# Optimization experiments

Hardware: AMD Instinct MI355X
Metric: run time of the kernel (lower is better)

## Reference

```python
import jax, jax.numpy as jnp
import numpy as np

V, D, NH, L, T, B = 32000, 1024, 16, 6, 1024, 2
HS = D // NH
EPS = 1e-5


def setup_inputs() -> dict:
    key = jax.random.key(0)
    ks = jax.random.split(key, 20)
    s = 0.02
    inp = {
        'tokens': jax.random.randint(ks[0], (B, T), 0, V),
        'tok_emb': jax.random.normal(ks[1], (V, D), jnp.float32) * s,
        'pos_emb': jax.random.normal(ks[2], (T, D), jnp.float32) * s,
        'Wq': jax.random.normal(ks[3], (L, D, NH, HS), jnp.float32) * s,
        'Wk': jax.random.normal(ks[4], (L, D, NH, HS), jnp.float32) * s,
        'Wv': jax.random.normal(ks[5], (L, D, NH, HS), jnp.float32) * s,
        'Wo': jax.random.normal(ks[6], (L, D, D), jnp.float32) * s,
        'bo': jnp.zeros((L, D), jnp.float32),
        'ln1_s': jnp.ones((L, D), jnp.float32),
        'ln1_b': jnp.zeros((L, D), jnp.float32),
        'ln2_s': jnp.ones((L, D), jnp.float32),
        'ln2_b': jnp.zeros((L, D), jnp.float32),
        'W1': jax.random.normal(ks[7], (L, D, 4 * D), jnp.float32) * s,
        'b1': jnp.zeros((L, 4 * D), jnp.float32),
        'W2': jax.random.normal(ks[8], (L, 4 * D, D), jnp.float32) * s,
        'b2': jnp.zeros((L, D), jnp.float32),
        'lnf_s': jnp.ones((D,), jnp.float32),
        'lnf_b': jnp.zeros((D,), jnp.float32),
        'Wlm': jax.random.normal(ks[9], (D, V), jnp.float32) * s,
        'blm': jnp.zeros((V,), jnp.float32),
    }
    return inp


def _layernorm(x, scale, bias):
    m = jnp.mean(x, axis=-1, keepdims=True)
    v = jnp.mean(jnp.square(x - m), axis=-1, keepdims=True)
    return (x - m) * jax.lax.rsqrt(v + EPS) * scale + bias


def reference(tokens, tok_emb, pos_emb, Wq, Wk, Wv, Wo, bo,
              ln1_s, ln1_b, ln2_s, ln2_b, W1, b1, W2, b2,
              lnf_s, lnf_b, Wlm, blm):
    x = tok_emb[tokens] + pos_emb[None, :, :]  # [B,T,D]
    causal = jnp.tril(jnp.ones((T, T), bool))
    scale = HS ** -0.5
    for l in range(L):
        h = _layernorm(x, ln1_s[l], ln1_b[l])
        q = jnp.einsum('btd,dhe->bhte', h, Wq[l])
        k = jnp.einsum('btd,dhe->bhte', h, Wk[l])
        v = jnp.einsum('btd,dhe->bhte', h, Wv[l])
        wei = jnp.einsum('bhqe,bhke->bhqk', q, k) * scale
        wei = jnp.where(causal, wei, -jnp.inf)
        wei = jax.nn.softmax(wei, axis=-1)
        attn = jnp.einsum('bhqk,bhke->bhqe', wei, v)  # [B,NH,T,HS]
        attn = attn.transpose(0, 2, 1, 3).reshape(B, T, D)
        x = x + attn @ Wo[l] + bo[l]
        h = _layernorm(x, ln2_s[l], ln2_b[l])
        x = x + jax.nn.relu(h @ W1[l] + b1[l]) @ W2[l] + b2[l]
    x = _layernorm(x, lnf_s, lnf_b)
    logits = x @ Wlm + blm  # [B,T,V]
    return logits
```

## Files before the change

kernel.cpp:

```cpp
#include <hip/hip_runtime.h>
#include <hip/hip_bf16.h>
#include <stdint.h>

#define L_LAYERS 6
#define D_MODEL  1024
#define N_HEAD   16
#define H_SZ     64
#define T_SEQ    1024
#define B_BATCH  2
#define M_ROWS   2048
#define V_VOCAB  32000

typedef __attribute__((ext_vector_type(8))) short bf16x8;
typedef __attribute__((ext_vector_type(4))) short bf16x4;
typedef __attribute__((ext_vector_type(4))) float floatx4;

static __device__ __forceinline__ short f2bf(float f) {
  __hip_bfloat16 h = __float2bfloat16(f);
  return *reinterpret_cast<short*>(&h);
}

static __device__ __forceinline__ void lds_cp16(const void* g, void* l) {
  __builtin_amdgcn_global_load_lds(
      (const __attribute__((address_space(1))) uint32_t*)g,
// ... 20 lines not shown
    int r = r0 + (p << 4);
    float4 v = *(const float4*)(ip + (size_t)r * C + c0);
    tile[r][c0] = v.x; tile[r][c0 + 1] = v.y; tile[r][c0 + 2] = v.z; tile[r][c0 + 3] = v.w;
  }
  __syncthreads();
  short* op = out + (size_t)(ct * 64) * R + rt * 64;
#pragma unroll
  for (int p = 0; p < 4; ++p) {
    int c = r0 + (p << 4);
    bf16x4 s;
    s.x = f2bf(tile[c0 + 0][c]);
    s.y = f2bf(tile[c0 + 1][c]);
    s.z = f2bf(tile[c0 + 2][c]);
    s.w = f2bf(tile[c0 + 3][c]);
    *(bf16x4*)(op + (size_t)c * R + c0) = s;
  }
}

__global__ __launch_bounds__(256) void embedln_kernel(const int* __restrict__ tokens,
                                                      const float* __restrict__ tok_emb,
                                                      const float* __restrict__ pos_emb,
                                                      float* __restrict__ x,
                                                      const float* __restrict__ sc,
                                                      const float* __restrict__ bi,
                                                      short* __restrict__ out) {
  int row = blockIdx.x, tid = threadIdx.x;
  int t = row & 1023;
  int tok = tokens[row];
  int c = tid << 2;
  float4 e = *(const float4*)(tok_emb + (size_t)tok * 1024 + c);
  float4 p = *(const float4*)(pos_emb + (size_t)t * 1024 + c);
  float4 v; v.x = e.x + p.x; v.y = e.y + p.y; v.z = e.z + p.z; v.w = e.w + p.w;
  *(float4*)(x + (size_t)row * 1024 + c) = v;
  float s = v.x + v.y + v.z + v.w;
  float q = v.x * v.x + v.y * v.y + v.z * v.z + v.w * v.w;
#pragma unroll
  for (int off = 32; off > 0; off >>= 1) {
    s += __shfl_xor(s, off);
    q += __shfl_xor(q, off);
  }
  __shared__ float rs[4], rq[4];
  if ((tid & 63) == 0) { rs[tid >> 6] = s; rq[tid >> 6] = q; }
  __syncthreads();
  s = rs[0] + rs[1] + rs[2] + rs[3];
  q = rq[0] + rq[1] + rq[2] + rq[3];
  float mean = s * (1.f / 1024.f);
  float var = q * (1.f / 1024.f) - mean * mean;
  float rstd = rsqrtf(var + 1e-5f);
  float4 g = *(const float4*)(sc + c);
  float4 bb = *(const float4*)(bi + c);
  bf16x4 o4;
  o4.x = f2bf((v.x - mean) * rstd * g.x + bb.x);
  o4.y = f2bf((v.y - mean) * rstd * g.y + bb.y);
  o4.z = f2bf((v.z - mean) * rstd * g.z + bb.z);
  o4.w = f2bf((v.w - mean) * rstd * g.w + bb.w);
  *(bf16x4*)(out + (size_t)row * 1024 + c) = o4;
}

__global__ __launch_bounds__(256) void lnred_kernel(float* __restrict__ xio,
                                                    const float* __restrict__ P0,
                                                    const float* __restrict__ P1,
                                                    const float* __restrict__ gb,
                                                    const float* __restrict__ sc,
                                                    const float* __restrict__ bi,
                                                    short* __restrict__ out) {
  int row = blockIdx.x, tid = threadIdx.x;
  int c = tid << 2;
  size_t base = (size_t)row * 1024 + c;
  float4 v = *(const float4*)(xio + base);
  float4 p0 = *(const float4*)(P0 + base);
  float4 p1 = *(const float4*)(P1 + base);
  float4 gv = *(const float4*)(gb + c);
  v.x += p0.x + p1.x + gv.x;
  v.y += p0.y + p1.y + gv.y;
  v.z += p0.z + p1.z + gv.z;
  v.w += p0.w + p1.w + gv.w;
  *(float4*)(xio + base) = v;
  float s = v.x + v.y + v.z + v.w;
  float q = v.x * v.x + v.y * v.y + v.z * v.z + v.w * v.w;
#pragma unroll
  for (int off = 32; off > 0; off >>= 1) {
    s += __shfl_xor(s, off);
    q += __shfl_xor(q, off);
  }
  __shared__ float rs[4], rq[4];
  if ((tid & 63) == 0) { rs[tid >> 6] = s; rq[tid >> 6] = q; }
  __syncthreads();
  s = rs[0] + rs[1] + rs[2] + rs[3];
  q = rq[0] + rq[1] + rq[2] + rq[3];
  float mean = s * (1.f / 1024.f);
  float var = q * (1.f / 1024.f) - mean * mean;
  float rstd = rsqrtf(var + 1e-5f);
  float4 g = *(const float4*)(sc + c);
  float4 bb = *(const float4*)(bi + c);
  bf16x4 o4;
  o4.x = f2bf((v.x - mean) * rstd * g.x + bb.x);
  o4.y = f2bf((v.y - mean) * rstd * g.y + bb.y);
  o4.z = f2bf((v.z - mean) * rstd * g.z + bb.z);
  o4.w = f2bf((v.w - mean) * rstd * g.w + bb.w);
  *(bf16x4*)(out + (size_t)row * 1024 + c) = o4;
}

__global__ __launch_bounds__(256) void lnred4_kernel(float* __restrict__ xio,
                                                     const float* __restrict__ P01,
                                                     const float* __restrict__ P23,
                                                     const float* __restrict__ gb,
                                                     const float* __restrict__ sc,
                                                     const float* __restrict__ bi,
                                                     short* __restrict__ out) {
  const size_t MN = (size_t)M_ROWS * 1024;
// ... 4 lines not shown
  float4 p0 = *(const float4*)(P01 + base);
  float4 p1 = *(const float4*)(P01 + MN + base);
  float4 p2 = *(const float4*)(P23 + base);
  float4 p3 = *(const float4*)(P23 + MN + base);
  float4 gv = *(const float4*)(gb + c);
  v.x += p0.x + p1.x + p2.x + p3.x + gv.x;
  v.y += p0.y + p1.y + p2.y + p3.y + gv.y;
  v.z += p0.z + p1.z + p2.z + p3.z + gv.z;
  v.w += p0.w + p1.w + p2.w + p3.w + gv.w;
  *(float4*)(xio + base) = v;
  float s = v.x + v.y + v.z + v.w;
  float q = v.x * v.x + v.y * v.y + v.z * v.z + v.w * v.w;
#pragma unroll
  for (int off = 32; off > 0; off >>= 1) {
    s += __shfl_xor(s, off);
    q += __shfl_xor(q, off);
  }
  __shared__ float rs[4], rq[4];
  if ((tid & 63) == 0) { rs[tid >> 6] = s; rq[tid >> 6] = q; }
  __syncthreads();
  s = rs[0] + rs[1] + rs[2] + rs[3];
  q = rq[0] + rq[1] + rq[2] + rq[3];
  float mean = s * (1.f / 1024.f);
  float var = q * (1.f / 1024.f) - mean * mean;
  float rstd = rsqrtf(var + 1e-5f);
  float4 g = *(const float4*)(sc + c);
  float4 bb = *(const float4*)(bi + c);
  bf16x4 o4;
  o4.x = f2bf((v.x - mean) * rstd * g.x + bb.x);
  o4.y = f2bf((v.y - mean) * rstd * g.y + bb.y);
  o4.z = f2bf((v.z - mean) * rstd * g.z + bb.z);
  o4.w = f2bf((v.w - mean) * rstd * g.w + bb.w);
  *(bf16x4*)(out + (size_t)row * 1024 + c) = o4;
}

__global__ __launch_bounds__(256) void gemm3sk_kernel(const short* __restrict__ A,
                                                      const short* __restrict__ Bt,
                                                      float* __restrict__ Pout,
                                                      int K, int N) {
  constexpr int ABY = 64 * 128;
  constexpr int BBY = 128 * 128;
  extern __shared__ char smem[];
  char* Asm = smem;
  char* Bsm = smem + 3 * ABY;
  const int NB = N >> 7;
  int nwg = 64 * NB;
  int bid = blockIdx.x;
  int wgid = (bid & 7) * (nwg >> 3) + (bid >> 3);
  int half = wgid >= (nwg >> 1);
  int w2 = wgid - half * (nwg >> 1);
  int bn = w2 >> 5, bm = w2 & 31;
  int kbase = half * (K >> 1);
  Pout += (size_t)half * M_ROWS * N;
  int tid = threadIdx.x;
  int lane = tid & 63, w = tid >> 6;
  int lr = lane & 15, lg = lane >> 4;
  int wn = w & 1, wm = w >> 1;

  const floatx4 FZ = {0.f, 0.f, 0.f, 0.f};
  floatx4 acc[2][4];
#pragma unroll
  for (int m = 0; m < 2; ++m)
#pragma unroll
    for (int n = 0; n < 4; ++n) acc[m][n] = FZ;

  size_t aoff[2], boff[4];
  {
    int rr = tid >> 3;
    int g = (tid & 7) ^ (rr & 7);
#pragma unroll
    for (int i = 0; i < 2; ++i)
      aoff[i] = (size_t)(bm * 64 + i * 32 + rr) * K + kbase + g * 8;
#pragma unroll
    for (int i = 0; i < 4; ++i)
      boff[i] = (size_t)(bn * 128 + i * 32 + rr) * K + kbase + g * 8;
  }

#define STA3(b, k0)                                                        \
  _Pragma("unroll") for (int i = 0; i < 2; ++i)                            \
    lds_cp16(A + aoff[i] + (k0), Asm + (b) * ABY + i * 4096 + tid * 16);
#define STB3(b, k0)                                                        \
  _Pragma("unroll") for (int i = 0; i < 4; ++i)                            \
    lds_cp16(Bt + boff[i] + (k0), Bsm + (b) * BBY + i * 4096 + tid * 16);
#define LDA3(b, kh)                                                        \
  _Pragma("unroll") for (int f = 0; f < 2; ++f) {                          \
    int lrow = wm * 32 + f * 16 + lr;                                      \
    af[f] = *(const bf16x8*)(Asm + (b) * ABY + lrow * 128 +                \
                             (((((kh) << 2) + lg) ^ (lrow & 7)) << 4));    \
  }
#define LDB3(b, kh)                                                        \
  _Pragma("unroll") for (int n = 0; n < 4; ++n) {                          \
    int lcol = wn * 64 + n * 16 + lr;                                      \
    bfr[n] = *(const bf16x8*)(Bsm + (b) * BBY + lcol * 128 +               \
                              (((((kh) << 2) + lg) ^ (lcol & 7)) << 4));   \
  }
#define MFMA3                                                              \
  __builtin_amdgcn_s_setprio(1);                                           \
  _Pragma("unroll") for (int f = 0; f < 2; ++f)                            \
  _Pragma("unroll") for (int n = 0; n < 4; ++n)                            \
    acc[f][n] = __builtin_amdgcn_mfma_f32_16x16x32_bf16(af[f], bfr[n],     \
                                                        acc[f][n], 0, 0, 0);\
  __builtin_amdgcn_s_setprio(0);

  const int nt = (K >> 1) >> 6;
  STA3(0, 0); STB3(0, 0);
  STA3(1, 64); STB3(1, 64);
  WVM(6);
  BARR;

  int cbuf = 0, sbuf = 2;
  for (int t = 0; t < nt; ++t) {
    bf16x8 af[2], bfr[4];
    bool pre = (t + 2 < nt);
    int k2 = (t + 2) << 6;
    if (pre) { STA3(sbuf, k2); }
    LDA3(cbuf, 0); LDB3(cbuf, 0);
    MFMA3;
    if (pre) { STB3(sbuf, k2); }
    LDA3(cbuf, 1); LDB3(cbuf, 1);
    MFMA3;
    if (pre) { WVM(6); } else { WVM(0); }
    BARR;
    cbuf = (cbuf == 2) ? 0 : cbuf + 1;
    sbuf = (sbuf == 2) ? 0 : sbuf + 1;
  }

#pragma unroll
  for (int n = 0; n < 4; ++n) {
    int col = (bn << 7) + wn * 64 + (n << 4) + lr;
#pragma unroll
    for (int m = 0; m < 2; ++m) {
      int row0 = bm * 64 + wm * 32 + (m << 4) + (lg << 2);
#pragma unroll
      for (int r = 0; r < 4; ++r)
        Pout[(size_t)(row0 + r) * N + col] = acc[m][n][r];
    }
  }
#undef STA3
#undef STB3
#undef LDA3
#undef LDB3
#undef MFMA3
}

template <bool BIAS, bool RELU, bool OUTBF16>
__global__ __launch_bounds__(512) void gemmw_kernel(const short* __restrict__ A,
                                                    const short* __restrict__ Bt,
                                                    const float* __restrict__ bias,
                                                    void* __restrict__ Cout,
                                                    int K, int N) {
  constexpr int ABY = 128 * 128;
  constexpr int BBY = 256 * 128;
  extern __shared__ char smem[];
  char* Asm = smem;
  char* Bsm = smem + 3 * ABY;
  const int NB = N >> 8;
  int nwg = 16 * NB;
  int bid = blockIdx.x;
  int wgid = (bid & 7) * (nwg >> 3) + (bid >> 3);
  int bn = wgid >> 4, bm = wgid & 15;
  int tid = threadIdx.x;
  int lane = tid & 63, w = tid >> 6;
  int lr = lane & 15, lg = lane >> 4;
  int wm = w >> 2, wn = w & 3;

  const floatx4 FZ = {0.f, 0.f, 0.f, 0.f};
  floatx4 acc[4][4];
#pragma unroll
  for (int m = 0; m < 4; ++m)
#pragma unroll
    for (int n = 0; n < 4; ++n) acc[m][n] = FZ;

  size_t aoff[2], boff[4];
  {
    int rr = tid >> 3;
    int g = (tid & 7) ^ (rr & 7);
#pragma unroll
    for (int i = 0; i < 2; ++i)
      aoff[i] = (size_t)(bm * 128 + i * 64 + rr) * K + g * 8;
#pragma unroll
    for (int i = 0; i < 4; ++i)
      boff[i] = (size_t)(bn * 256 + i * 64 + rr) * K + g * 8;
// ... 26 lines not shown
  __builtin_amdgcn_s_setprio(0);

  const int nt = K >> 6;
  STAW(0, 0); STBW(0, 0);
  STAW(1, 64); STBW(1, 64);
  WVM(6);
  BARR;

  int cbuf = 0, sbuf = 2;
  for (int t = 0; t < nt; ++t) {
    bf16x8 af[4], bfr[4];
    bool pre = (t + 2 < nt);
    int k2 = (t + 2) << 6;
    if (pre) { STAW(sbuf, k2); }
    LDAW(cbuf, 0); LDBW(cbuf, 0);
    MFMAW;
    if (pre) { STBW(sbuf, k2); }
    LDAW(cbuf, 1); LDBW(cbuf, 1);
    MFMAW;
    if (pre) { WVM(6); } else { WVM(0); }
    BARR;
    cbuf = (cbuf == 2) ? 0 : cbuf + 1;
    sbuf = (sbuf == 2) ? 0 : sbuf + 1;
  }

#pragma unroll
  for (int n = 0; n < 4; ++n) {
    int col = (bn << 8) + wn * 64 + (n << 4) + lr;
    float bv = 0.f;
    if (BIAS) bv = bias[col];
#pragma unroll
    for (int m = 0; m < 4; ++m) {
      int row0 = bm * 128 + wm * 64 + (m << 4) + (lg << 2);
#pragma unroll
      for (int r = 0; r < 4; ++r) {
        size_t idx = (size_t)(row0 + r) * N + col;
        float val = acc[m][n][r] + bv;
        if (RELU) val = fmaxf(val, 0.f);
        if (OUTBF16) ((short*)Cout)[idx] = f2bf(val);
        else ((float*)Cout)[idx] = val;
      }
    }
  }
#undef STAW
#undef STBW
#undef LDAW
#undef LDBW
#undef MFMAW
}

__global__ __launch_bounds__(512) void gemmwsk_kernel(const short* __restrict__ A,
                                                      const short* __restrict__ Bt,
                                                      float* __restrict__ P01,
                                                      float* __restrict__ P23,
                                                      int K, int N) {
  constexpr int ABY = 128 * 128;
  constexpr int BBY = 256 * 128;
  extern __shared__ char smem[];
  char* Asm = smem;
  char* Bsm = smem + 3 * ABY;
  const int NB = N >> 8;
  int nwg = 16 * NB * 4;
  int bid = blockIdx.x;
  int wgid = (bid & 7) * (nwg >> 3) + (bid >> 3);
  int per = nwg >> 2;
  int part = wgid / per;
  int w2 = wgid - part * per;
  int bn = w2 >> 4, bm = w2 & 15;
  int kbase = part * (K >> 2);
  float* Pout = (part < 2 ? P01 + (size_t)part * M_ROWS * N
                          : P23 + (size_t)(part - 2) * M_ROWS * N);
  int tid = threadIdx.x;
  int lane = tid & 63, w = tid >> 6;
// ... 196 lines not shown
  LDA8(0, 1); LDB8(1);
  MFMA16(0, 1);
  WVM(0);
  BARR;
  LDA8(1, 0);
  MFMA16(1, 0);
  LDA8(1, 1);
  MFMA16(1, 1);

#pragma unroll
  for (int n = 0; n < 4; ++n) {
    int col = (bn << 8) + (wn << 6) + (n << 4) + lr;
    float bv = 0.f;
    if (BIAS) bv = bias[col];
#pragma unroll
    for (int m = 0; m < 8; ++m) {
      int row0 = (bm << 8) + (wm << 7) + (m << 4) + (lg << 2);
#pragma unroll
      for (int r = 0; r < 4; ++r) {
        size_t idx = (size_t)(row0 + r) * N + col;
        float val = acc[m][n][r] + bv;
        if (OUTBF16) ((short*)Cout)[idx] = f2bf(val);
        else ((float*)Cout)[idx] = val;
      }
    }
  }
#undef LDA8
#undef LDB8
#undef MFMA16
#undef STA8
#undef STB8
}

__global__ __launch_bounds__(256) void vt_kernel(const short* __restrict__ qkv,
                                                 short* __restrict__ vt) {
  int bh = blockIdx.x, tt = blockIdx.y;
  int b = bh >> 4, hh = bh & 15;
  __shared__ short tile[64][68];
  int tid = threadIdx.x;
  int r0 = tid >> 4;
  int c4 = (tid & 15) << 2;
  const short* ip = qkv + (size_t)((b << 10) + (tt << 6)) * 3072 + 2048 + (hh << 6);
#pragma unroll
  for (int p = 0; p < 4; ++p) {
    int t = r0 + (p << 4);
    bf16x4 v = *(const bf16x4*)(ip + (size_t)t * 3072 + c4);
    tile[t][c4] = v.x; tile[t][c4 + 1] = v.y; tile[t][c4 + 2] = v.z; tile[t][c4 + 3] = v.w;
  }
  __syncthreads();
  short* op = vt + (size_t)(bh << 6) * 1024 + (tt << 6);
#pragma unroll
  for (int p = 0; p < 4; ++p) {
    int e = r0 + (p << 4);
    bf16x4 sv;
    sv.x = tile[c4 + 0][e];
    sv.y = tile[c4 + 1][e];
    sv.z = tile[c4 + 2][e];
    sv.w = tile[c4 + 3][e];
    *(bf16x4*)(op + (size_t)e * 1024 + c4) = sv;
  }
}

__global__ __launch_bounds__(256) void attn_kernel(const short* __restrict__ qkv,
                                                   const short* __restrict__ vt,
                                                   short* __restrict__ out) {
  int bh = blockIdx.x;
  int qt = blockIdx.y;
  int b = bh >> 4, hh = bh & 15;
  int tid = threadIdx.x;
  int lane = tid & 63, w = tid >> 6;
  int lr = lane & 15, lg = lane >> 4;

  __shared__ short Ks[64 * 64];
  __shared__ short Vs[64 * 64];
  __shared__ short Ps[4][16 * 68];

  const floatx4 FZ = {0.f, 0.f, 0.f, 0.f};
  const short* qb = qkv + (size_t)((b << 10) + (qt << 6) + (w << 4) + lr) * 3072 + (hh << 6);
  bf16x8 qf0 = *(const bf16x8*)(qb + (lg << 3));
  bf16x8 qf1 = *(const bf16x8*)(qb + 32 + (lg << 3));

  floatx4 o[4];
  float mrun[4], lrun[4];
#pragma unroll
  for (int r = 0; r < 4; ++r) { o[r] = FZ; mrun[r] = -3e38f; lrun[r] = 0.f; }

  int sr = lane >> 3;
  int cb = (lane & 7) << 4;
  int csw = cb ^ (sr << 4);
  const short* kB = qkv + (size_t)(b << 10) * 3072 + 1024 + (hh << 6);
  const short* vB = vt + (size_t)(bh << 6) * 1024;

  for (int jt = 0; jt <= qt; ++jt) {
    __syncthreads();
#pragma unroll
    for (int j = 0; j < 2; ++j) {
      int ch = w * 2 + j;
      int row = (ch << 3) + sr;
      lds_cp16(kB + (size_t)((jt << 6) + row) * 3072 + (csw >> 1), (short*)Ks + (ch << 9));
      lds_cp16(vB + (size_t)row * 1024 + (jt << 6) + (csw >> 1), (short*)Vs + (ch << 9));
    }
    __syncthreads();

    const char* KsB = (const char*)Ks;
    const char* VsB = (const char*)Vs;
    floatx4 s[4];
#pragma unroll
    for (int f = 0; f < 4; ++f) {
      int rk = (f << 4) + lr;
      int sw = (rk & 7) << 4;
      bf16x8 kf0 = *(const bf16x8*)(KsB + rk * 128 + ((lg << 4) ^ sw));
      bf16x8 kf1 = *(const bf16x8*)(KsB + rk * 128 + ((64 + (lg << 4)) ^ sw));
      floatx4 t = __builtin_amdgcn_mfma_f32_16x16x32_bf16(qf0, kf0, FZ, 0, 0, 0);
      s[f] = __builtin_amdgcn_mfma_f32_16x16x32_bf16(qf1, kf1, t, 0, 0, 0);
    }

    float p[4][4], mt[4];
    bool diag = (jt == qt);
    int rowloc = (w << 4) + (lg << 2);
#pragma unroll
    for (int r = 0; r < 4; ++r) {
      float m = -3e38f;
#pragma unroll
      for (int f = 0; f < 4; ++f) {
        float sv = s[f][r] * 0.125f;
        if (diag && ((f << 4) + lr > rowloc + r)) sv = -3e38f;
        p[f][r] = sv;
        m = fmaxf(m, sv);
      }
      mt[r] = m;
    }
#pragma unroll
    for (int off = 1; off < 16; off <<= 1) {
#pragma unroll
      for (int r = 0; r < 4; ++r) mt[r] = fmaxf(mt[r], __shfl_xor(mt[r], off));
    }
    float corr[4], psum[4];
#pragma unroll
    for (int r = 0; r < 4; ++r) {
      float mnew = fmaxf(mrun[r], mt[r]);
      corr[r] = __expf(mrun[r] - mnew);
      mrun[r] = mnew;
      float ps = 0.f;
#pragma unroll
      for (int f = 0; f < 4; ++f) {
        float e = __expf(p[f][r] - mnew);
        p[f][r] = e;
        ps += e;
      }
      psum[r] = ps;
    }
#pragma unroll
    for (int off = 1; off < 16; off <<= 1) {
#pragma unroll
      for (int r = 0; r < 4; ++r) psum[r] += __shfl_xor(psum[r], off);
    }
    floatx4 cv;
#pragma unroll
    for (int r = 0; r < 4; ++r) { lrun[r] = lrun[r] * corr[r] + psum[r]; cv[r] = corr[r]; }
#pragma unroll
    for (int f = 0; f < 4; ++f) o[f] *= cv;

    char* PsB = (char*)&Ps[w][0];
#pragma unroll
    for (int f = 0; f < 4; ++f)
#pragma unroll
      for (int r = 0; r < 4; ++r)
        *(short*)(PsB + ((lg << 2) + r) * 136 + (((f << 4) + lr) << 1)) = f2bf(p[f][r]);

#pragma unroll
    for (int kk = 0; kk < 2; ++kk) {
      const char* pb = PsB + lr * 136 + (kk << 6) + (lg << 4);
      union { struct { bf16x4 lo, hi; } h2; bf16x8 v; } pu;
      pu.h2.lo = *(const bf16x4*)pb;
      pu.h2.hi = *(const bf16x4*)(pb + 8);
      bf16x8 pa = pu.v;
#pragma unroll
      for (int f = 0; f < 4; ++f) {
        int rv = (f << 4) + lr;
        int sw = (rv & 7) << 4;
        bf16x8 vf = *(const bf16x8*)(VsB + rv * 128 + ((((kk << 6)) + (lg << 4)) ^ sw));
        o[f] = __builtin_amdgcn_mfma_f32_16x16x32_bf16(pa, vf, o[f], 0, 0, 0);
      }
    }
  }

#pragma unroll
  for (int f = 0; f < 4; ++f) {
#pragma unroll
    for (int r = 0; r < 4; ++r) {
      int row = (qt << 6) + (w << 4) + (lg << 2) + r;
      int col = (hh << 6) + (f << 4) + lr;
      out[(size_t)((b << 10) + row) * 1024 + col] = f2bf(o[f][r] / lrun[r]);
    }
  }
}

extern "C" void kernel_launch(void* const* d_in, const int* in_sizes, int n_in,
                              void* d_out, int out_size, void* d_ws, size_t ws_size,
                              hipStream_t stream) {
  const int*   tokens  = (const int*)d_in[0];
  const float* tok_emb = (const float*)d_in[1];
  const float* pos_emb = (const float*)d_in[2];
  const float* Wq  = (const float*)d_in[3];
  const float* Wk  = (const float*)d_in[4];
  const float* Wv  = (const float*)d_in[5];
  const float* Wo  = (const float*)d_in[6];
  const float* bo  = (const float*)d_in[7];
  const float* ln1s = (const float*)d_in[8];
  const float* ln1b = (const float*)d_in[9];
  const float* ln2s = (const float*)d_in[10];
  const float* ln2b = (const float*)d_in[11];
  const float* W1  = (const float*)d_in[12];
  const float* b1  = (const float*)d_in[13];
  const float* W2  = (const float*)d_in[14];
  const float* b2  = (const float*)d_in[15];
  const float* lnfs = (const float*)d_in[16];
  const float* lnfb = (const float*)d_in[17];
  const float* Wlm = (const float*)d_in[18];
  const float* blm = (const float*)d_in[19];

  short* wqkvT = (short*)d_ws;
  short* woT   = wqkvT + (size_t)L_LAYERS * 3072 * 1024;
  short* w1T   = woT   + (size_t)L_LAYERS * 1024 * 1024;
  short* w2T   = w1T   + (size_t)L_LAYERS * 4096 * 1024;
  short* wlmT  = w2T   + (size_t)L_LAYERS * 1024 * 4096;
  float* x     = (float*)(wlmT + (size_t)V_VOCAB * 1024);
  short* h     = (short*)(x + (size_t)M_ROWS * 1024);
  short* qkv   = h + (size_t)M_ROWS * 1024;
  short* vtb   = qkv + (size_t)M_ROWS * 3072;
  short* attnb = vtb + (size_t)B_BATCH * N_HEAD * H_SZ * T_SEQ;
  short* mid   = attnb + (size_t)M_ROWS * 1024;
  float* psum  = (float*)(mid + (size_t)M_ROWS * 4096);
  float* psum1 = psum + (size_t)M_ROWS * 1024;
  float* psum23 = (float*)qkv;

  dim3 blk(256, 1, 1);

  (void)hipFuncSetAttribute(reinterpret_cast<const void*>(&gemm8_kernel<true, false>),
                            hipFuncAttributeMaxDynamicSharedMemorySize, 131072);
  (void)hipFuncSetAttribute(reinterpret_cast<const void*>(&gemm3sk_kernel),
                            hipFuncAttributeMaxDynamicSharedMemorySize, 73728);
  (void)hipFuncSetAttribute(reinterpret_cast<const void*>(&gemmw_kernel<false, false, true>),
                            hipFuncAttributeMaxDynamicSharedMemorySize, 147456);
  (void)hipFuncSetAttribute(reinterpret_cast<const void*>(&gemmw_kernel<true, true, true>),
                            hipFuncAttributeMaxDynamicSharedMemorySize, 147456);
  (void)hipFuncSetAttribute(reinterpret_cast<const void*>(&gemmwsk_kernel),
                            hipFuncAttributeMaxDynamicSharedMemorySize, 147456);

  transpose_cvt<<<dim3(16, 16, 6), blk, 0, stream>>>(Wq, wqkvT,             1024, 1024, 1048576, 3072 * 1024);
  transpose_cvt<<<dim3(16, 16, 6), blk, 0, stream>>>(Wk, wqkvT + 1048576,   1024, 1024, 1048576, 3072 * 1024);
  transpose_cvt<<<dim3(16, 16, 6), blk, 0, stream>>>(Wv, wqkvT + 2097152,   1024, 1024, 1048576, 3072 * 1024);
  transpose_cvt<<<dim3(16, 16, 6), blk, 0, stream>>>(Wo, woT,               1024, 1024, 1048576, 1048576);
  transpose_cvt<<<dim3(16, 64, 6), blk, 0, stream>>>(W1, w1T,               1024, 4096, 4194304, 4194304);
  transpose_cvt<<<dim3(64, 16, 6), blk, 0, stream>>>(W2, w2T,               4096, 1024, 4194304, 4194304);
  transpose_cvt<<<dim3(16, 500, 1), blk, 0, stream>>>(Wlm, wlmT,            1024, V_VOCAB, 0, 0);

  embedln_kernel<<<M_ROWS, blk, 0, stream>>>(tokens, tok_emb, pos_emb, x, ln1s, ln1b, h);

  for (int l = 0; l < L_LAYERS; ++l) {
    if (l > 0) {
      lnred4_kernel<<<M_ROWS, blk, 0, stream>>>(x, psum, psum23, b2 + (l - 1) * 1024,
                                                ln1s + l * 1024, ln1b + l * 1024, h);
    }
    gemmw_kernel<false, false, true><<<16 * 12, dim3(512, 1, 1), 147456, stream>>>(
        h, wqkvT + (size_t)l * 3072 * 1024, nullptr, qkv, 1024, 3072);
    vt_kernel<<<dim3(32, 16), blk, 0, stream>>>(qkv, vtb);
    attn_kernel<<<dim3(32, 16), blk, 0, stream>>>(qkv, vtb, attnb);
    gemm3sk_kernel<<<64 * 8, blk, 73728, stream>>>(
        attnb, woT + (size_t)l * 1048576, psum, 1024, 1024);
    lnred_kernel<<<M_ROWS, blk, 0, stream>>>(x, psum, psum1, bo + l * 1024,
                                             ln2s + l * 1024, ln2b + l * 1024, h);
    gemmw_kernel<true, true, true><<<16 * 16, dim3(512, 1, 1), 147456, stream>>>(
        h, w1T + (size_t)l * 4194304, b1 + l * 4096, mid, 1024, 4096);
    gemmwsk_kernel<<<16 * 16, dim3(512, 1, 1), 147456, stream>>>(
        mid, w2T + (size_t)l * 4194304, psum, psum23, 4096, 1024);
  }

  lnred4_kernel<<<M_ROWS, blk, 0, stream>>>(x, psum, psum23, b2 + 5 * 1024,
                                            lnfs, lnfb, h);
  gemm8_kernel<true, false><<<dim3(8 * 125), dim3(512, 1, 1), 131072, stream>>>(
      h, wlmT, blm, (float*)d_out, 1024, V_VOCAB);
}
```

Measured before the change: 1.075 ms.

## Double-buffer attention K/V loads, use exp2 softmax, reuse split-K GEMM for Wo

The attention kernel now double-buffers its K and V tiles in LDS. It issues async global-to-LDS copies for the next key block while computing the current one, replacing the two full barriers around each synchronous load. Softmax folds log2(e) into the score scale and uses exp2f instead of __expf. The output projection drops the dedicated 2-way split-K gemm3sk kernel and reuses the wider gemmwsk kernel with 4 K-partials written to psum/psum23, followed by lnred4 instead of lnred. This trades more partial-sum traffic and doubled attention LDS for better latency hiding and fewer distinct kernel variants.

```diff
diff --git a/kernel.cpp b/kernel.cpp
--- a/kernel.cpp
+++ b/kernel.cpp
@@ -76,50 +76,6 @@
   float4 p = *(const float4*)(pos_emb + (size_t)t * 1024 + c);
   float4 v; v.x = e.x + p.x; v.y = e.y + p.y; v.z = e.z + p.z; v.w = e.w + p.w;
   *(float4*)(x + (size_t)row * 1024 + c) = v;
-  float s = v.x + v.y + v.z + v.w;
-  float q = v.x * v.x + v.y * v.y + v.z * v.z + v.w * v.w;
-#pragma unroll
-  for (int off = 32; off > 0; off >>= 1) {
-    s += __shfl_xor(s, off);
-    q += __shfl_xor(q, off);
-  }
-  __shared__ float rs[4], rq[4];
-  if ((tid & 63) == 0) { rs[tid >> 6] = s; rq[tid >> 6] = q; }
-  __syncthreads();
-  s = rs[0] + rs[1] + rs[2] + rs[3];
-  q = rq[0] + rq[1] + rq[2] + rq[3];
-  float mean = s * (1.f / 1024.f);
-  float var = q * (1.f / 1024.f) - mean * mean;
-  float rstd = rsqrtf(var + 1e-5f);
-  float4 g = *(const float4*)(sc + c);
-  float4 bb = *(const float4*)(bi + c);
-  bf16x4 o4;
-  o4.x = f2bf((v.x - mean) * rstd * g.x + bb.x);
-  o4.y = f2bf((v.y - mean) * rstd * g.y + bb.y);
-  o4.z = f2bf((v.z - mean) * rstd * g.z + bb.z);
-  o4.w = f2bf((v.w - mean) * rstd * g.w + bb.w);
-  *(bf16x4*)(out + (size_t)row * 1024 + c) = o4;
-}
-
-__global__ __launch_bounds__(256) void lnred_kernel(float* __restrict__ xio,
-                                                    const float* __restrict__ P0,
-                                                    const float* __restrict__ P1,
-                                                    const float* __restrict__ gb,
-                                                    const float* __restrict__ sc,
-                                                    const float* __restrict__ bi,
-                                                    short* __restrict__ out) {
-  int row = blockIdx.x, tid = threadIdx.x;
-  int c = tid << 2;
-  size_t base = (size_t)row * 1024 + c;
-  float4 v = *(const float4*)(xio + base);
-  float4 p0 = *(const float4*)(P0 + base);
-  float4 p1 = *(const float4*)(P1 + base);
-  float4 gv = *(const float4*)(gb + c);
-  v.x += p0.x + p1.x + gv.x;
-  v.y += p0.y + p1.y + gv.y;
-  v.z += p0.z + p1.z + gv.z;
-  v.w += p0.w + p1.w + gv.w;
-  *(float4*)(xio + base) = v;
   float s = v.x + v.y + v.z + v.w;
   float q = v.x * v.x + v.y * v.y + v.z * v.z + v.w * v.w;
 #pragma unroll
@@ -190,115 +146,6 @@
   o4.z = f2bf((v.z - mean) * rstd * g.z + bb.z);
   o4.w = f2bf((v.w - mean) * rstd * g.w + bb.w);
   *(bf16x4*)(out + (size_t)row * 1024 + c) = o4;
-}
-
-__global__ __launch_bounds__(256) void gemm3sk_kernel(const short* __restrict__ A,
-                                                      const short* __restrict__ Bt,
-                                                      float* __restrict__ Pout,
-                                                      int K, int N) {
-  constexpr int ABY = 64 * 128;
-  constexpr int BBY = 128 * 128;
-  extern __shared__ char smem[];
-  char* Asm = smem;
-  char* Bsm = smem + 3 * ABY;
-  const int NB = N >> 7;
-  int nwg = 64 * NB;
-  int bid = blockIdx.x;
-  int wgid = (bid & 7) * (nwg >> 3) + (bid >> 3);
-  int half = wgid >= (nwg >> 1);
-  int w2 = wgid - half * (nwg >> 1);
-  int bn = w2 >> 5, bm = w2 & 31;
-  int kbase = half * (K >> 1);
-  Pout += (size_t)half * M_ROWS * N;
-  int tid = threadIdx.x;
-  int lane = tid & 63, w = tid >> 6;
-  int lr = lane & 15, lg = lane >> 4;
-  int wn = w & 1, wm = w >> 1;
-
-  const floatx4 FZ = {0.f, 0.f, 0.f, 0.f};
-  floatx4 acc[2][4];
-#pragma unroll
-  for (int m = 0; m < 2; ++m)
-#pragma unroll
-    for (int n = 0; n < 4; ++n) acc[m][n] = FZ;
-
-  size_t aoff[2], boff[4];
-  {
-    int rr = tid >> 3;
-    int g = (tid & 7) ^ (rr & 7);
-#pragma unroll
-    for (int i = 0; i < 2; ++i)
-      aoff[i] = (size_t)(bm * 64 + i * 32 + rr) * K + kbase + g * 8;
-#pragma unroll
-    for (int i = 0; i < 4; ++i)
-      boff[i] = (size_t)(bn * 128 + i * 32 + rr) * K + kbase + g * 8;
-  }
-
-#define STA3(b, k0)                                                        \
-  _Pragma("unroll") for (int i = 0; i < 2; ++i)                            \
-    lds_cp16(A + aoff[i] + (k0), Asm + (b) * ABY + i * 4096 + tid * 16);
-#define STB3(b, k0)                                                        \
-  _Pragma("unroll") for (int i = 0; i < 4; ++i)                            \
-    lds_cp16(Bt + boff[i] + (k0), Bsm + (b) * BBY + i * 4096 + tid * 16);
-#define LDA3(b, kh)                                                        \
-  _Pragma("unroll") for (int f = 0; f < 2; ++f) {                          \
-    int lrow = wm * 32 + f * 16 + lr;                                      \
-    af[f] = *(const bf16x8*)(Asm + (b) * ABY + lrow * 128 +                \
-                             (((((kh) << 2) + lg) ^ (lrow & 7)) << 4));    \
-  }
-#define LDB3(b, kh)                                                        \
-  _Pragma("unroll") for (int n = 0; n < 4; ++n) {                          \
-    int lcol = wn * 64 + n * 16 + lr;                                      \
-    bfr[n] = *(const bf16x8*)(Bsm + (b) * BBY + lcol * 128 +               \
-                              (((((kh) << 2) + lg) ^ (lcol & 7)) << 4));   \
-  }
-#define MFMA3                                                              \
-  __builtin_amdgcn_s_setprio(1);                                           \
-  _Pragma("unroll") for (int f = 0; f < 2; ++f)                            \
-  _Pragma("unroll") for (int n = 0; n < 4; ++n)                            \
-    acc[f][n] = __builtin_amdgcn_mfma_f32_16x16x32_bf16(af[f], bfr[n],     \
-                                                        acc[f][n], 0, 0, 0);\
-  __builtin_amdgcn_s_setprio(0);
-
-  const int nt = (K >> 1) >> 6;
-  STA3(0, 0); STB3(0, 0);
-  STA3(1, 64); STB3(1, 64);
-  WVM(6);
-  BARR;
-
-  int cbuf = 0, sbuf = 2;
-  for (int t = 0; t < nt; ++t) {
-    bf16x8 af[2], bfr[4];
-    bool pre = (t + 2 < nt);
-    int k2 = (t + 2) << 6;
-    if (pre) { STA3(sbuf, k2); }
-    LDA3(cbuf, 0); LDB3(cbuf, 0);
-    MFMA3;
-    if (pre) { STB3(sbuf, k2); }
-    LDA3(cbuf, 1); LDB3(cbuf, 1);
-    MFMA3;
-    if (pre) { WVM(6); } else { WVM(0); }
-    BARR;
-    cbuf = (cbuf == 2) ? 0 : cbuf + 1;
-    sbuf = (sbuf == 2) ? 0 : sbuf + 1;
-  }
-
-#pragma unroll
-  for (int n = 0; n < 4; ++n) {
-    int col = (bn << 7) + wn * 64 + (n << 4) + lr;
-#pragma unroll
-    for (int m = 0; m < 2; ++m) {
-      int row0 = bm * 64 + wm * 32 + (m << 4) + (lg << 2);
-#pragma unroll
-      for (int r = 0; r < 4; ++r)
-        Pout[(size_t)(row0 + r) * N + col] = acc[m][n][r];
-    }
-  }
-#undef STA3
-#undef STB3
-#undef LDA3
-#undef LDB3
-#undef MFMA3
 }
 
 template <bool BIAS, bool RELU, bool OUTBF16>
@@ -706,11 +553,12 @@
   int lane = tid & 63, w = tid >> 6;
   int lr = lane & 15, lg = lane >> 4;
 
-  __shared__ short Ks[64 * 64];
-  __shared__ short Vs[64 * 64];
+  __shared__ short Ks[2][64 * 64];
+  __shared__ short Vs[2][64 * 64];
   __shared__ short Ps[4][16 * 68];
 
   const floatx4 FZ = {0.f, 0.f, 0.f, 0.f};
+  const float C2 = 0.18033688f;
   const short* qb = qkv + (size_t)((b << 10) + (qt << 6) + (w << 4) + lr) * 3072 + (hh << 6);
   bf16x8 qf0 = *(const bf16x8*)(qb + (lg << 3));
   bf16x8 qf1 = *(const bf16x8*)(qb + 32 + (lg << 3));
@@ -726,19 +574,26 @@
   const short* kB = qkv + (size_t)(b << 10) * 3072 + 1024 + (hh << 6);
   const short* vB = vt + (size_t)(bh << 6) * 1024;
 
+#define STKV(jt, bb)                                                       \
+  _Pragma("unroll") for (int j = 0; j < 2; ++j) {                          \
+    int ch = w * 2 + j;                                                    \
+    int row = (ch << 3) + sr;                                              \
+    lds_cp16(kB + (size_t)(((jt) << 6) + row) * 3072 + (csw >> 1),         \
+             (short*)Ks + (bb) * 4096 + (ch << 9));                        \
+    lds_cp16(vB + (size_t)row * 1024 + ((jt) << 6) + (csw >> 1),           \
+             (short*)Vs + (bb) * 4096 + (ch << 9));                        \
+  }
+
+  STKV(0, 0);
+  WVM(0);
+  BARR;
+
+  int buf = 0;
   for (int jt = 0; jt <= qt; ++jt) {
-    __syncthreads();
-#pragma unroll
-    for (int j = 0; j < 2; ++j) {
-      int ch = w * 2 + j;
-      int row = (ch << 3) + sr;
-      lds_cp16(kB + (size_t)((jt << 6) + row) * 3072 + (csw >> 1), (short*)Ks + (ch << 9));
-      lds_cp16(vB + (size_t)row * 1024 + (jt << 6) + (csw >> 1), (short*)Vs + (ch << 9));
-    }
-    __syncthreads();
-
-    const char* KsB = (const char*)Ks;
-    const char* VsB = (const char*)Vs;
+    if (jt < qt) { STKV(jt + 1, buf ^ 1); }
+
+    const char* KsB = (const char*)Ks + (buf << 13);
+    const char* VsB = (const char*)Vs + (buf << 13);
     floatx4 s[4];
 #pragma unroll
     for (int f = 0; f < 4; ++f) {
@@ -758,7 +613,7 @@
       float m = -3e38f;
 #pragma unroll
       for (int f = 0; f < 4; ++f) {
-        float sv = s[f][r] * 0.125f;
+        float sv = s[f][r] * C2;
         if (diag && ((f << 4) + lr > rowloc + r)) sv = -3e38f;
         p[f][r] = sv;
         m = fmaxf(m, sv);
@@ -774,12 +629,12 @@
 #pragma unroll
     for (int r = 0; r < 4; ++r) {
       float mnew = fmaxf(mrun[r], mt[r]);
-      corr[r] = __expf(mrun[r] - mnew);
+      corr[r] = exp2f(mrun[r] - mnew);
       mrun[r] = mnew;
       float ps = 0.f;
 #pragma unroll
       for (int f = 0; f < 4; ++f) {
-        float e = __expf(p[f][r] - mnew);
+        float e = exp2f(p[f][r] - mnew);
         p[f][r] = e;
         ps += e;
       }
@@ -818,7 +673,12 @@
         o[f] = __builtin_amdgcn_mfma_f32_16x16x32_bf16(pa, vf, o[f], 0, 0, 0);
       }
     }
-  }
+
+    WVM(0);
+    BARR;
+    buf ^= 1;
+  }
+#undef STKV
 
 #pragma unroll
   for (int f = 0; f < 4; ++f) {
@@ -867,15 +727,12 @@
   short* attnb = vtb + (size_t)B_BATCH * N_HEAD * H_SZ * T_SEQ;
   short* mid   = attnb + (size_t)M_ROWS * 1024;
   float* psum  = (float*)(mid + (size_t)M_ROWS * 4096);
-  float* psum1 = psum + (size_t)M_ROWS * 1024;
   float* psum23 = (float*)qkv;
 
   dim3 blk(256, 1, 1);
 
   (void)hipFuncSetAttribute(reinterpret_cast<const void*>(&gemm8_kernel<true, false>),
                             hipFuncAttributeMaxDynamicSharedMemorySize, 131072);
-  (void)hipFuncSetAttribute(reinterpret_cast<const void*>(&gemm3sk_kernel),
-                            hipFuncAttributeMaxDynamicSharedMemorySize, 73728);
   (void)hipFuncSetAttribute(reinterpret_cast<const void*>(&gemmw_kernel<false, false, true>),
                             hipFuncAttributeMaxDynamicSharedMemorySize, 147456);
   (void)hipFuncSetAttribute(reinterpret_cast<const void*>(&gemmw_kernel<true, true, true>),
@@ -902,10 +759,10 @@
         h, wqkvT + (size_t)l * 3072 * 1024, nullptr, qkv, 1024, 3072);
     vt_kernel<<<dim3(32, 16), blk, 0, stream>>>(qkv, vtb);
     attn_kernel<<<dim3(32, 16), blk, 0, stream>>>(qkv, vtb, attnb);
-    gemm3sk_kernel<<<64 * 8, blk, 73728, stream>>>(
-        attnb, woT + (size_t)l * 1048576, psum, 1024, 1024);
-    lnred_kernel<<<M_ROWS, blk, 0, stream>>>(x, psum, psum1, bo + l * 1024,
-                                             ln2s + l * 1024, ln2b + l * 1024, h);
+    gemmwsk_kernel<<<16 * 4 * 4, dim3(512, 1, 1), 147456, stream>>>(
+        attnb, woT + (size_t)l * 1048576, psum, psum23, 1024, 1024);
+    lnred4_kernel<<<M_ROWS, blk, 0, stream>>>(x, psum, psum23, bo + l * 1024,
+                                              ln2s + l * 1024, ln2b + l * 1024, h);
     gemmw_kernel<true, true, true><<<16 * 16, dim3(512, 1, 1), 147456, stream>>>(
         h, w1T + (size_t)l * 4194304, b1 + l * 4096, mid, 1024, 4096);
     gemmwsk_kernel<<<16 * 16, dim3(512, 1, 1), 147456, stream>>>(
```

Result: slower. 1.117 ms (+3.9%).

## Double-buffer K/V tiles in attention and switch softmax to exp2

Applied to the files above, without the earlier changes.

The attention kernel now holds two K/V LDS buffers. It issues the async global-to-LDS load for the next key tile before computing on the current one, with a single wait and barrier per iteration in place of two barriers. The softmax scale is folded into log2e so exp2f replaces __expf. This is meant to hide global load latency behind the MFMA work, at the cost of doubled LDS use, which may reduce occupancy.

```diff
diff --git a/kernel.cpp b/kernel.cpp
--- a/kernel.cpp
+++ b/kernel.cpp
@@ -706,11 +706,12 @@
   int lane = tid & 63, w = tid >> 6;
   int lr = lane & 15, lg = lane >> 4;
 
-  __shared__ short Ks[64 * 64];
-  __shared__ short Vs[64 * 64];
+  __shared__ short Ks[2][64 * 64];
+  __shared__ short Vs[2][64 * 64];
   __shared__ short Ps[4][16 * 68];
 
   const floatx4 FZ = {0.f, 0.f, 0.f, 0.f};
+  const float C2 = 0.18033688f;
   const short* qb = qkv + (size_t)((b << 10) + (qt << 6) + (w << 4) + lr) * 3072 + (hh << 6);
   bf16x8 qf0 = *(const bf16x8*)(qb + (lg << 3));
   bf16x8 qf1 = *(const bf16x8*)(qb + 32 + (lg << 3));
@@ -726,19 +727,26 @@
   const short* kB = qkv + (size_t)(b << 10) * 3072 + 1024 + (hh << 6);
   const short* vB = vt + (size_t)(bh << 6) * 1024;
 
+#define STKV(jt, bb)                                                       \
+  _Pragma("unroll") for (int j = 0; j < 2; ++j) {                          \
+    int ch = w * 2 + j;                                                    \
+    int row = (ch << 3) + sr;                                              \
+    lds_cp16(kB + (size_t)(((jt) << 6) + row) * 3072 + (csw >> 1),         \
+             (short*)Ks + (bb) * 4096 + (ch << 9));                        \
+    lds_cp16(vB + (size_t)row * 1024 + ((jt) << 6) + (csw >> 1),           \
+             (short*)Vs + (bb) * 4096 + (ch << 9));                        \
+  }
+
+  STKV(0, 0);
+  WVM(0);
+  BARR;
+
+  int buf = 0;
   for (int jt = 0; jt <= qt; ++jt) {
-    __syncthreads();
-#pragma unroll
-    for (int j = 0; j < 2; ++j) {
-      int ch = w * 2 + j;
-      int row = (ch << 3) + sr;
-      lds_cp16(kB + (size_t)((jt << 6) + row) * 3072 + (csw >> 1), (short*)Ks + (ch << 9));
-      lds_cp16(vB + (size_t)row * 1024 + (jt << 6) + (csw >> 1), (short*)Vs + (ch << 9));
-    }
-    __syncthreads();
-
-    const char* KsB = (const char*)Ks;
-    const char* VsB = (const char*)Vs;
+    if (jt < qt) { STKV(jt + 1, buf ^ 1); }
+
+    const char* KsB = (const char*)Ks + (buf << 13);
+    const char* VsB = (const char*)Vs + (buf << 13);
     floatx4 s[4];
 #pragma unroll
     for (int f = 0; f < 4; ++f) {
@@ -758,7 +766,7 @@
       float m = -3e38f;
 #pragma unroll
       for (int f = 0; f < 4; ++f) {
-        float sv = s[f][r] * 0.125f;
+        float sv = s[f][r] * C2;
         if (diag && ((f << 4) + lr > rowloc + r)) sv = -3e38f;
         p[f][r] = sv;
         m = fmaxf(m, sv);
@@ -774,12 +782,12 @@
 #pragma unroll
     for (int r = 0; r < 4; ++r) {
       float mnew = fmaxf(mrun[r], mt[r]);
-      corr[r] = __expf(mrun[r] - mnew);
+      corr[r] = exp2f(mrun[r] - mnew);
       mrun[r] = mnew;
       float ps = 0.f;
 #pragma unroll
       for (int f = 0; f < 4; ++f) {
-        float e = __expf(p[f][r] - mnew);
+        float e = exp2f(p[f][r] - mnew);
         p[f][r] = e;
         ps += e;
       }
@@ -818,7 +826,12 @@
         o[f] = __builtin_amdgcn_mfma_f32_16x16x32_bf16(pa, vf, o[f], 0, 0, 0);
       }
     }
-  }
+
+    WVM(0);
+    BARR;
+    buf ^= 1;
+  }
+#undef STKV
 
 #pragma unroll
   for (int f = 0; f < 4; ++f) {
```

Result: no change. 1.094 ms (+1.8%).

## Fuse V transpose into QKV GEMM epilogue and widen attention KV tiles

Applied to the files above, without the earlier changes.

The QKV GEMM epilogue now writes the V columns directly in transposed per-head layout, which removes the separate vt_kernel launch and its round trip through memory. The attention kernel now processes 128-key tiles instead of 64, with new XOR swizzles on the K and V shared-memory tiles. It also folds the softmax scale into a log2e constant so it can use exp2f. The wider tile halves loop iterations and barriers but raises shared-memory use and register pressure, and the transposed V stores from the GEMM epilogue are strided 8-byte writes.

```diff
diff --git a/kernel.cpp b/kernel.cpp
--- a/kernel.cpp
+++ b/kernel.cpp
@@ -301,11 +301,12 @@
 #undef MFMA3
 }
 
-template <bool BIAS, bool RELU, bool OUTBF16>
+template <bool BIAS, bool RELU, bool OUTBF16, bool VSPLIT>
 __global__ __launch_bounds__(512) void gemmw_kernel(const short* __restrict__ A,
                                                     const short* __restrict__ Bt,
                                                     const float* __restrict__ bias,
                                                     void* __restrict__ Cout,
+                                                    short* __restrict__ vtb,
                                                     int K, int N) {
   constexpr int ABY = 128 * 128;
   constexpr int BBY = 256 * 128;
@@ -398,13 +399,24 @@
 #pragma unroll
     for (int m = 0; m < 4; ++m) {
       int row0 = bm * 128 + wm * 64 + (m << 4) + (lg << 2);
-#pragma unroll
-      for (int r = 0; r < 4; ++r) {
-        size_t idx = (size_t)(row0 + r) * N + col;
-        float val = acc[m][n][r] + bv;
-        if (RELU) val = fmaxf(val, 0.f);
-        if (OUTBF16) ((short*)Cout)[idx] = f2bf(val);
-        else ((float*)Cout)[idx] = val;
+      if (VSPLIT && col >= 2048) {
+        int hc = col - 2048;
+        int brow = row0 >> 10, t0 = row0 & 1023;
+        ushort4 pk;
+        pk.x = (unsigned short)f2bf(acc[m][n][0]);
+        pk.y = (unsigned short)f2bf(acc[m][n][1]);
+        pk.z = (unsigned short)f2bf(acc[m][n][2]);
+        pk.w = (unsigned short)f2bf(acc[m][n][3]);
+        *(ushort4*)(vtb + ((size_t)(((brow << 4) + (hc >> 6)) << 6) + (hc & 63)) * 1024 + t0) = pk;
+      } else {
+#pragma unroll
+        for (int r = 0; r < 4; ++r) {
+          size_t idx = (size_t)(row0 + r) * N + col;
+          float val = acc[m][n][r] + bv;
+          if (RELU) val = fmaxf(val, 0.f);
+          if (OUTBF16) ((short*)Cout)[idx] = f2bf(val);
+          else ((float*)Cout)[idx] = val;
+        }
       }
     }
   }
@@ -667,35 +679,6 @@
 #undef STB8
 }
 
-__global__ __launch_bounds__(256) void vt_kernel(const short* __restrict__ qkv,
-                                                 short* __restrict__ vt) {
-  int bh = blockIdx.x, tt = blockIdx.y;
-  int b = bh >> 4, hh = bh & 15;
-  __shared__ short tile[64][68];
-  int tid = threadIdx.x;
-  int r0 = tid >> 4;
-  int c4 = (tid & 15) << 2;
-  const short* ip = qkv + (size_t)((b << 10) + (tt << 6)) * 3072 + 2048 + (hh << 6);
-#pragma unroll
-  for (int p = 0; p < 4; ++p) {
-    int t = r0 + (p << 4);
-    bf16x4 v = *(const bf16x4*)(ip + (size_t)t * 3072 + c4);
-    tile[t][c4] = v.x; tile[t][c4 + 1] = v.y; tile[t][c4 + 2] = v.z; tile[t][c4 + 3] = v.w;
-  }
-  __syncthreads();
-  short* op = vt + (size_t)(bh << 6) * 1024 + (tt << 6);
-#pragma unroll
-  for (int p = 0; p < 4; ++p) {
-    int e = r0 + (p << 4);
-    bf16x4 sv;
-    sv.x = tile[c4 + 0][e];
-    sv.y = tile[c4 + 1][e];
-    sv.z = tile[c4 + 2][e];
-    sv.w = tile[c4 + 3][e];
-    *(bf16x4*)(op + (size_t)e * 1024 + c4) = sv;
-  }
-}
-
 __global__ __launch_bounds__(256) void attn_kernel(const short* __restrict__ qkv,
                                                    const short* __restrict__ vt,
                                                    short* __restrict__ out) {
@@ -706,11 +689,12 @@
   int lane = tid & 63, w = tid >> 6;
   int lr = lane & 15, lg = lane >> 4;
 
-  __shared__ short Ks[64 * 64];
-  __shared__ short Vs[64 * 64];
-  __shared__ short Ps[4][16 * 68];
+  __shared__ short Ks[128 * 64];
+  __shared__ short Vs[64 * 128];
+  __shared__ short Ps[4][16 * 132];
 
   const floatx4 FZ = {0.f, 0.f, 0.f, 0.f};
+  const float C2 = 0.18033688f;
   const short* qb = qkv + (size_t)((b << 10) + (qt << 6) + (w << 4) + lr) * 3072 + (hh << 6);
   bf16x8 qf0 = *(const bf16x8*)(qb + (lg << 3));
   bf16x8 qf1 = *(const bf16x8*)(qb + 32 + (lg << 3));
@@ -720,76 +704,91 @@
 #pragma unroll
   for (int r = 0; r < 4; ++r) { o[r] = FZ; mrun[r] = -3e38f; lrun[r] = 0.f; }
 
-  int sr = lane >> 3;
-  int cb = (lane & 7) << 4;
-  int csw = cb ^ (sr << 4);
+  int krow = tid >> 3, kgr = tid & 7;
+  int vrow = tid >> 4, vgr = tid & 15;
   const short* kB = qkv + (size_t)(b << 10) * 3072 + 1024 + (hh << 6);
   const short* vB = vt + (size_t)(bh << 6) * 1024;
 
-  for (int jt = 0; jt <= qt; ++jt) {
-    __syncthreads();
-#pragma unroll
-    for (int j = 0; j < 2; ++j) {
-      int ch = w * 2 + j;
-      int row = (ch << 3) + sr;
-      lds_cp16(kB + (size_t)((jt << 6) + row) * 3072 + (csw >> 1), (short*)Ks + (ch << 9));
-      lds_cp16(vB + (size_t)row * 1024 + (jt << 6) + (csw >> 1), (short*)Vs + (ch << 9));
-    }
-    __syncthreads();
+  const int nc = (qt + 2) >> 1;
+  for (int jt = 0; jt < nc; ++jt) {
+#pragma unroll
+    for (int i = 0; i < 4; ++i) {
+      int r = (i << 5) + krow;
+      lds_cp16(kB + (size_t)((jt << 7) + r) * 3072 + ((kgr ^ (r & 7)) << 3),
+               (char*)Ks + i * 4096 + tid * 16);
+    }
+#pragma unroll
+    for (int i = 0; i < 4; ++i) {
+      int r = (i << 4) + vrow;
+      lds_cp16(vB + (size_t)r * 1024 + (jt << 7) + ((vgr ^ (r & 15)) << 3),
+               (char*)Vs + i * 4096 + tid * 16);
+    }
+    WVM(0);
+    BARR;
 
     const char* KsB = (const char*)Ks;
     const char* VsB = (const char*)Vs;
-    floatx4 s[4];
-#pragma unroll
-    for (int f = 0; f < 4; ++f) {
+    floatx4 s[8];
+#pragma unroll
+    for (int f = 0; f < 8; ++f) {
       int rk = (f << 4) + lr;
-      int sw = (rk & 7) << 4;
-      bf16x8 kf0 = *(const bf16x8*)(KsB + rk * 128 + ((lg << 4) ^ sw));
-      bf16x8 kf1 = *(const bf16x8*)(KsB + rk * 128 + ((64 + (lg << 4)) ^ sw));
-      floatx4 t = __builtin_amdgcn_mfma_f32_16x16x32_bf16(qf0, kf0, FZ, 0, 0, 0);
-      s[f] = __builtin_amdgcn_mfma_f32_16x16x32_bf16(qf1, kf1, t, 0, 0, 0);
-    }
-
-    float p[4][4], mt[4];
-    bool diag = (jt == qt);
-    int rowloc = (w << 4) + (lg << 2);
-#pragma unroll
-    for (int r = 0; r < 4; ++r) {
-      float m = -3e38f;
-#pragma unroll
-      for (int f = 0; f < 4; ++f) {
-        float sv = s[f][r] * 0.125f;
-        if (diag && ((f << 4) + lr > rowloc + r)) sv = -3e38f;
-        p[f][r] = sv;
-        m = fmaxf(m, sv);
-      }
-      mt[r] = m;
-    }
-#pragma unroll
-    for (int off = 1; off < 16; off <<= 1) {
+      int sw = rk & 7;
+      bf16x8 kf0 = *(const bf16x8*)(KsB + rk * 128 + ((lg ^ sw) << 4));
+      bf16x8 kf1 = *(const bf16x8*)(KsB + rk * 128 + (((4 + lg) ^ sw) << 4));
+      floatx4 t0 = __builtin_amdgcn_mfma_f32_16x16x32_bf16(qf0, kf0, FZ, 0, 0, 0);
+      s[f] = __builtin_amdgcn_mfma_f32_16x16x32_bf16(qf1, kf1, t0, 0, 0, 0);
+    }
+
+    bool last = (jt == nc - 1);
+    int qrow0 = (qt << 6) + (w << 4) + (lg << 2);
+    int kvb = (jt << 7) + lr;
+    if (last) {
+#pragma unroll
+      for (int f = 0; f < 8; ++f)
+#pragma unroll
+        for (int r = 0; r < 4; ++r) {
+          float sv = s[f][r] * C2;
+          if (kvb + (f << 4) > qrow0 + r) sv = -3e38f;
+          s[f][r] = sv;
+        }
+    } else {
+#pragma unroll
+      for (int f = 0; f < 8; ++f)
+#pragma unroll
+        for (int r = 0; r < 4; ++r) s[f][r] *= C2;
+    }
+
+    float mt[4];
+#pragma unroll
+    for (int r = 0; r < 4; ++r) mt[r] = -3e38f;
+#pragma unroll
+    for (int f = 0; f < 8; ++f)
+#pragma unroll
+      for (int r = 0; r < 4; ++r) mt[r] = fmaxf(mt[r], s[f][r]);
+#pragma unroll
+    for (int off = 1; off < 16; off <<= 1)
 #pragma unroll
       for (int r = 0; r < 4; ++r) mt[r] = fmaxf(mt[r], __shfl_xor(mt[r], off));
-    }
+
     float corr[4], psum[4];
 #pragma unroll
     for (int r = 0; r < 4; ++r) {
       float mnew = fmaxf(mrun[r], mt[r]);
-      corr[r] = __expf(mrun[r] - mnew);
+      corr[r] = exp2f(mrun[r] - mnew);
       mrun[r] = mnew;
       float ps = 0.f;
 #pragma unroll
-      for (int f = 0; f < 4; ++f) {
-        float e = __expf(p[f][r] - mnew);
-        p[f][r] = e;
+      for (int f = 0; f < 8; ++f) {
+        float e = exp2f(s[f][r] - mnew);
+        s[f][r] = e;
         ps += e;
       }
       psum[r] = ps;
     }
 #pragma unroll
-    for (int off = 1; off < 16; off <<= 1) {
+    for (int off = 1; off < 16; off <<= 1)
 #pragma unroll
       for (int r = 0; r < 4; ++r) psum[r] += __shfl_xor(psum[r], off);
-    }
     floatx4 cv;
 #pragma unroll
     for (int r = 0; r < 4; ++r) { lrun[r] = lrun[r] * corr[r] + psum[r]; cv[r] = corr[r]; }
@@ -798,14 +797,14 @@
 
     char* PsB = (char*)&Ps[w][0];
 #pragma unroll
-    for (int f = 0; f < 4; ++f)
+    for (int f = 0; f < 8; ++f)
 #pragma unroll
       for (int r = 0; r < 4; ++r)
-        *(short*)(PsB + ((lg << 2) + r) * 136 + (((f << 4) + lr) << 1)) = f2bf(p[f][r]);
-
-#pragma unroll
-    for (int kk = 0; kk < 2; ++kk) {
-      const char* pb = PsB + lr * 136 + (kk << 6) + (lg << 4);
+        *(short*)(PsB + ((lg << 2) + r) * 264 + (((f << 4) + lr) << 1)) = f2bf(s[f][r]);
+
+#pragma unroll
+    for (int kk = 0; kk < 4; ++kk) {
+      const char* pb = PsB + lr * 264 + (kk << 6) + (lg << 4);
       union { struct { bf16x4 lo, hi; } h2; bf16x8 v; } pu;
       pu.h2.lo = *(const bf16x4*)pb;
       pu.h2.hi = *(const bf16x4*)(pb + 8);
@@ -813,11 +812,11 @@
 #pragma unroll
       for (int f = 0; f < 4; ++f) {
         int rv = (f << 4) + lr;
-        int sw = (rv & 7) << 4;
-        bf16x8 vf = *(const bf16x8*)(VsB + rv * 128 + ((((kk << 6)) + (lg << 4)) ^ sw));
+        bf16x8 vf = *(const bf16x8*)(VsB + rv * 256 + ((((kk << 2) + lg) ^ (rv & 15)) << 4));
         o[f] = __builtin_amdgcn_mfma_f32_16x16x32_bf16(pa, vf, o[f], 0, 0, 0);
       }
     }
+    BARR;
   }
 
 #pragma unroll
@@ -876,9 +875,9 @@
                             hipFuncAttributeMaxDynamicSharedMemorySize, 131072);
   (void)hipFuncSetAttribute(reinterpret_cast<const void*>(&gemm3sk_kernel),
                             hipFuncAttributeMaxDynamicSharedMemorySize, 73728);
-  (void)hipFuncSetAttribute(reinterpret_cast<const void*>(&gemmw_kernel<false, false, true>),
+  (void)hipFuncSetAttribute(reinterpret_cast<const void*>(&gemmw_kernel<false, false, true, true>),
                             hipFuncAttributeMaxDynamicSharedMemorySize, 147456);
-  (void)hipFuncSetAttribute(reinterpret_cast<const void*>(&gemmw_kernel<true, true, true>),
+  (void)hipFuncSetAttribute(reinterpret_cast<const void*>(&gemmw_kernel<true, true, true, false>),
                             hipFuncAttributeMaxDynamicSharedMemorySize, 147456);
   (void)hipFuncSetAttribute(reinterpret_cast<const void*>(&gemmwsk_kernel),
                             hipFuncAttributeMaxDynamicSharedMemorySize, 147456);
@@ -898,16 +897,15 @@
       lnred4_kernel<<<M_ROWS, blk, 0, stream>>>(x, psum, psum23, b2 + (l - 1) * 1024,
                                                 ln1s + l * 1024, ln1b + l * 1024, h);
     }
-    gemmw_kernel<false, false, true><<<16 * 12, dim3(512, 1, 1), 147456, stream>>>(
-        h, wqkvT + (size_t)l * 3072 * 1024, nullptr, qkv, 1024, 3072);
-    vt_kernel<<<dim3(32, 16), blk, 0, stream>>>(qkv, vtb);
+    gemmw_kernel<false, false, true, true><<<16 * 12, dim3(512, 1, 1), 147456, stream>>>(
+        h, wqkvT + (size_t)l * 3072 * 1024, nullptr, qkv, vtb, 1024, 3072);
     attn_kernel<<<dim3(32, 16), blk, 0, stream>>>(qkv, vtb, attnb);
     gemm3sk_kernel<<<64 * 8, blk, 73728, stream>>>(
         attnb, woT + (size_t)l * 1048576, psum, 1024, 1024);
     lnred_kernel<<<M_ROWS, blk, 0, stream>>>(x, psum, psum1, bo + l * 1024,
                                              ln2s + l * 1024, ln2b + l * 1024, h);
-    gemmw_kernel<true, true, true><<<16 * 16, dim3(512, 1, 1), 147456, stream>>>(
-        h, w1T + (size_t)l * 4194304, b1 + l * 4096, mid, 1024, 4096);
+    gemmw_kernel<true, true, true, false><<<16 * 16, dim3(512, 1, 1), 147456, stream>>>(
+        h, w1T + (size_t)l * 4194304, b1 + l * 4096, mid, nullptr, 1024, 4096);
     gemmwsk_kernel<<<16 * 16, dim3(512, 1, 1), 147456, stream>>>(
         mid, w2T + (size_t)l * 4194304, psum, psum23, 4096, 1024);
   }
```

New measurement: 1.046 ms. -2.7%, faster.
